# Performance work log

Hardware: AMD Instinct MI355X
Metric: run time of the kernel (lower is better)

The kernel has to match this reference:

```python
import jax, jax.numpy as jnp
import numpy as np

N_NODES = 100_000
N_EDGES = 1_600_000
D_IN, D_HID, D_OUT = 256, 64, 32
NUM_PROP = 10
ALPHA = 0.1


def setup_inputs() -> dict:
    key = jax.random.key(0)
    ks = jax.random.split(key, 8)
    features = jax.random.normal(ks[0], (N_NODES, D_IN), dtype=jnp.float32)
    row = jax.random.randint(ks[1], (N_EDGES,), 0, N_NODES, dtype=jnp.int32)
    col = jax.random.randint(ks[2], (N_EDGES,), 0, N_NODES, dtype=jnp.int32)
    # positive edge weights (stand-in for symmetric-normalized adjacency values)
    edge_vals = jax.random.uniform(ks[3], (N_EDGES,), dtype=jnp.float32) / 16.0
    W1 = jax.random.normal(ks[4], (D_IN, D_HID), dtype=jnp.float32) / np.sqrt(D_IN)
    b1 = jnp.zeros((D_HID,), dtype=jnp.float32)
    W2 = jax.random.normal(ks[5], (D_HID, D_OUT), dtype=jnp.float32) / np.sqrt(D_HID)
    b2 = jnp.zeros((D_OUT,), dtype=jnp.float32)
    return {"features": features, "row": row, "col": col, "edge_vals": edge_vals,
            "W1": W1, "b1": b1, "W2": W2, "b2": b2}


def _spmm(row, col, vals, x):
    # COO sparse-dense matmul: out[r] += vals[e] * x[col[e]] for each edge e
    return jax.ops.segment_sum(vals[:, None] * x[col], row, num_segments=N_NODES)


def reference(features, row, col, edge_vals, W1, b1, W2, b2):
    # head_transform: 2-layer MLP
    x = jax.nn.relu(features @ W1 + b1) @ W2 + b2  # [N, D_OUT]
    x0 = x
    # APPNP propagation: x = (1-alpha) * (A @ x) + alpha * x0
    def body(_, x):
        return (1.0 - ALPHA) * _spmm(row, col, edge_vals, x) + ALPHA * x0
    x = jax.lax.fori_loop(0, NUM_PROP, body, x)
    return x
```

## Files before the change

kernel.cpp:

```cpp
#include <hip/hip_runtime.h>

#define N_NODES 100000
#define N_EDGES 1600000
#define D_IN    256
#define D_HID   64
#define D_OUT   32
#define NPROP   10

#define NBUCK 196
#define CHUNK 6080
#define NCHUNK ((N_EDGES + CHUNK - 1) / CHUNK)

typedef _Float16 half_t;
typedef _Float16 h8  __attribute__((ext_vector_type(8)));
typedef _Float16 h4  __attribute__((ext_vector_type(4)));
typedef float    f4v __attribute__((ext_vector_type(4)));

__global__ __launch_bounds__(256) void pack_kernel(
    const float* __restrict__ W1, const float* __restrict__ W2,
    half_t* __restrict__ W1T, half_t* __restrict__ W2T)
{
  int t = blockIdx.x * 256 + threadIdx.x;
  if (t < 64 * 256) { int n = t >> 8, k = t & 255; W1T[t] = (half_t)W1[k * 64 + n]; }
  if (t < 32 * 64)  { int n = t >> 6, k = t & 63;  W2T[t] = (half_t)W2[k * 32 + n]; }
}

#define HSTRIDE 72

__global__ __launch_bounds__(256) void mlp_kernel(
    const float* __restrict__ F, const half_t* __restrict__ W1T,
    const float* __restrict__ b1, const half_t* __restrict__ W2T,
    const float* __restrict__ b2, half_t* __restrict__ x0h)
{
  __shared__ half_t h_lds[16 * HSTRIDE];
  __shared__ half_t out_lds[16 * 32];
  int t = threadIdx.x;
  int w = t >> 6, lane = t & 63;
  int m = lane & 15, q = lane >> 4;
  int node0 = blockIdx.x * 16;
  int hid0 = w * 16;

  f4v acc = {0.f, 0.f, 0.f, 0.f};
  const float* arow = F + (size_t)(node0 + m) * D_IN + q * 8;
  const half_t* brow = W1T + (size_t)(hid0 + m) * D_IN + q * 8;
#pragma unroll
  for (int s = 0; s < 8; ++s) {
    float4 f0 = *(const float4*)(arow + s * 32);
    float4 f1 = *(const float4*)(arow + s * 32 + 4);
    h8 a;
    a[0] = (_Float16)f0.x; a[1] = (_Float16)f0.y;
    a[2] = (_Float16)f0.z; a[3] = (_Float16)f0.w;
    a[4] = (_Float16)f1.x; a[5] = (_Float16)f1.y;
    a[6] = (_Float16)f1.z; a[7] = (_Float16)f1.w;
    h8 b = *(const h8*)(brow + s * 32);
    acc = __builtin_amdgcn_mfma_f32_16x16x32_f16(a, b, acc, 0, 0, 0);
  }

  {
    int col = hid0 + m;
    float bb = b1[col];
#pragma unroll
    for (int i = 0; i < 4; ++i) {
      float hv = fmaxf(acc[i] + bb, 0.f);
      h_lds[(q * 4 + i) * HSTRIDE + col] = (half_t)hv;
    }
  }
  __syncthreads();

  if (w < 2) {
    f4v acc2 = {0.f, 0.f, 0.f, 0.f};
    int out0 = w * 16;
#pragma unroll
    for (int s = 0; s < 2; ++s) {
      h8 a = *(const h8*)(h_lds + m * HSTRIDE + s * 32 + q * 8);
      h8 b = *(const h8*)(W2T + (size_t)(out0 + m) * D_HID + s * 32 + q * 8);
      acc2 = __builtin_amdgcn_mfma_f32_16x16x32_f16(a, b, acc2, 0, 0, 0);
    }
    int oc = out0 + m;
    float b2v = b2[oc];
#pragma unroll
    for (int i = 0; i < 4; ++i)
      out_lds[(q * 4 + i) * 32 + oc] = (half_t)(acc2[i] + b2v);
  }
  __syncthreads();

  if (t < 64) {
    int nl = t >> 2, qq = t & 3;
    *(int4*)(x0h + (size_t)(node0 + nl) * D_OUT + qq * 8) =
        *(const int4*)(out_lds + nl * 32 + qq * 8);
  }
}

__global__ __launch_bounds__(256) void bhist_kernel(
    const int* __restrict__ row, int* __restrict__ bcnt)
{
  __shared__ int lb[NBUCK];
  int t = threadIdx.x;
  for (int i = t; i < NBUCK; i += 256) lb[i] = 0;
  __syncthreads();
  int stride = gridDim.x * 256;
  for (int e = blockIdx.x * 256 + t; e < N_EDGES; e += stride)
    atomicAdd(&lb[row[e] >> 9], 1);
  __syncthreads();
  for (int i = t; i < NBUCK; i += 256)
    if (lb[i]) atomicAdd(&bcnt[i], lb[i]);
}

__global__ __launch_bounds__(256) void bscan_kernel(
    const int* __restrict__ bcnt, int* __restrict__ bbase, int* __restrict__ pbase)
{
  __shared__ int l1[256], l2[256];
  int t = threadIdx.x;
  int a = (t < NBUCK) ? bcnt[t] : 0;
  int r = (t < NBUCK) ? (((a + 3) & ~3) + 3 * 512) : 0;
  l1[t] = a; l2[t] = r;
  __syncthreads();
  for (int off = 1; off < 256; off <<= 1) {
    int x1 = (t >= off) ? l1[t - off] : 0;
    int x2 = (t >= off) ? l2[t - off] : 0;
    __syncthreads();
    l1[t] += x1; l2[t] += x2;
    __syncthreads();
  }
  if (t < NBUCK) { bbase[t] = l1[t] - a; pbase[t] = l2[t] - r; }
  if (t == NBUCK - 1) { bbase[NBUCK] = l1[t]; pbase[NBUCK] = l2[t]; }
}

__global__ __launch_bounds__(256) void bscatter_kernel(
    const int* __restrict__ row, const int* __restrict__ col,
    const float* __restrict__ vals, int* __restrict__ bfill,
    const int* __restrict__ bbase, int2* __restrict__ ebuck)
{
  __shared__ int2 img[CHUNK];
  __shared__ unsigned short sbk[CHUNK];
  __shared__ int cnt[NBUCK], base[NBUCK], gb[NBUCK], fil[NBUCK];
  __shared__ int ssc[256];
  int t = threadIdx.x;
  int e0 = blockIdx.x * CHUNK;
  int n = min(CHUNK, N_EDGES - e0);

  for (int i = t; i < NBUCK; i += 256) { cnt[i] = 0; fil[i] = 0; }
  __syncthreads();
  for (int i = t; i < n; i += 256) atomicAdd(&cnt[row[e0 + i] >> 9], 1);
  __syncthreads();
  int c = (t < NBUCK) ? cnt[t] : 0;
  ssc[t] = c;
  __syncthreads();
  for (int off = 1; off < 256; off <<= 1) {
    int add = (t >= off) ? ssc[t - off] : 0;
    __syncthreads();
    ssc[t] += add;
    __syncthreads();
  }
  if (t < NBUCK) {
    base[t] = ssc[t] - c;
    gb[t] = c ? atomicAdd(&bfill[t], c) : 0;
  }
  __syncthreads();
  for (int i = t; i < n; i += 256) {
    int r = row[e0 + i];
    int bk = r >> 9;
    int p = base[bk] + atomicAdd(&fil[bk], 1);
    img[p] = make_int2(col[e0 + i] | ((r & 511) << 17),
                       __float_as_int(vals[e0 + i]));
    sbk[p] = (unsigned short)bk;
  }
  __syncthreads();
  for (int i = t; i < n; i += 256) {
    int bk = sbk[i];
    ebuck[bbase[bk] + gb[bk] + (i - base[bk])] = img[i];
  }
}

__global__ __launch_bounds__(256) void bsort_kernel(
    const int* __restrict__ bbase, const int* __restrict__ pbase,
    const int2* __restrict__ ebuck, int2* __restrict__ epack,
    int* __restrict__ row_ptr)
{
  __shared__ int acnt[512], loff[513], lfill[512], ssc[256];
  int b = blockIdx.x, t = threadIdx.x;
  int r0 = b * 512;
  int nr = min(512, N_NODES - r0);
  int eb = bbase[b];
  int ne = bbase[b + 1] - eb;
  int pb = pbase[b];

  acnt[t] = 0; acnt[t + 256] = 0;
  lfill[t] = 0; lfill[t + 256] = 0;
  __syncthreads();
  for (int i = t; i < ne; i += 256)
    atomicAdd(&acnt[((unsigned)ebuck[eb + i].x) >> 17], 1);
  __syncthreads();
  int i0 = 2 * t, i1 = 2 * t + 1;
  int a0 = acnt[i0], a1 = acnt[i1];
  int p0 = (a0 + 3) & ~3, p1 = (a1 + 3) & ~3;
  int s = p0 + p1;
  ssc[t] = s;
  __syncthreads();
  for (int off = 1; off < 256; off <<= 1) {
    int add = (t >= off) ? ssc[t - off] : 0;
    __syncthreads();
    ssc[t] += add;
    __syncthreads();
  }
  int ex = ssc[t] - s;
  loff[i0] = ex;
  loff[i1] = ex + p0;
  if (t == 255) loff[512] = ssc[255];
  __syncthreads();
  int T = ssc[255];
  int slack = (pbase[b + 1] - pb) - T;
  int units = min(slack >> 2, nr);
  if (i0 < nr) row_ptr[r0 + i0] = pb + loff[i0] + 4 * min(i0, units);
  if (i1 < nr) row_ptr[r0 + i1] = pb + loff[i1] + 4 * min(i1, units);
  if (b == NBUCK - 1 && t == 0)
    row_ptr[N_NODES] = pb + loff[nr] + 4 * units;
  __syncthreads();
  for (int i = t; i < ne; i += 256) {
    int2 ed = ebuck[eb + i];
    int lr = ((unsigned)ed.x) >> 17;
    int cl = ed.x & 0x1FFFF;
    int p = loff[lr] + 4 * min(lr, units) + atomicAdd(&lfill[lr], 1);
    epack[pb + p] = make_int2(cl, ed.y);
  }
  __syncthreads();
  for (int i = t; i < nr; i += 256) {
    int a = acnt[i];
    int size_i = ((a + 3) & ~3) + 4 * (i < units);
    int st = loff[i] + 4 * min(i, units);
    for (int p = st + a; p < st + size_i; ++p)
      epack[pb + p] = make_int2(0, 0);
  }
}

__global__ __launch_bounds__(256) void spmm_kernel(
    const int* __restrict__ rp, const int2* __restrict__ ep,
    const half_t* __restrict__ xin, const half_t* __restrict__ x0h,
    half_t* __restrict__ xout, float* __restrict__ fout, int last)
{
  int gt = blockIdx.x * 256 + threadIdx.x;
  int r = gt >> 3;
  int c4 = (gt & 7) * 4;
  if (r >= N_NODES) return;
  int e0 = rp[r], e1 = rp[r + 1];

  float acc[4] = {0.f, 0.f, 0.f, 0.f};
  for (int e = e0; e < e1; e += 4) {
    int2 p0 = ep[e];
    int2 p1 = ep[e + 1];
    int2 p2 = ep[e + 2];
    int2 p3 = ep[e + 3];
    h4 g0 = *(const h4*)(xin + (size_t)p0.x * D_OUT + c4);
    h4 g1 = *(const h4*)(xin + (size_t)p1.x * D_OUT + c4);
    h4 g2 = *(const h4*)(xin + (size_t)p2.x * D_OUT + c4);
    h4 g3 = *(const h4*)(xin + (size_t)p3.x * D_OUT + c4);
    float v0 = __int_as_float(p0.y);
    float v1 = __int_as_float(p1.y);
    float v2 = __int_as_float(p2.y);
    float v3 = __int_as_float(p3.y);
#pragma unroll
    for (int j = 0; j < 4; ++j) {
      acc[j] = fmaf(v0, (float)g0[j], acc[j]);
      acc[j] = fmaf(v1, (float)g1[j], acc[j]);
      acc[j] = fmaf(v2, (float)g2[j], acc[j]);
      acc[j] = fmaf(v3, (float)g3[j], acc[j]);
    }
  }

  h4 x0v = *(const h4*)(x0h + (size_t)r * D_OUT + c4);
  if (last) {
    float4 o;
    o.x = 0.9f * acc[0] + 0.1f * (float)x0v[0];
    o.y = 0.9f * acc[1] + 0.1f * (float)x0v[1];
    o.z = 0.9f * acc[2] + 0.1f * (float)x0v[2];
    o.w = 0.9f * acc[3] + 0.1f * (float)x0v[3];
    *(float4*)(fout + (size_t)r * D_OUT + c4) = o;
  } else {
    h4 o;
#pragma unroll
    for (int j = 0; j < 4; ++j)
      o[j] = (half_t)(0.9f * acc[j] + 0.1f * (float)x0v[j]);
    *(h4*)(xout + (size_t)r * D_OUT + c4) = o;
  }
}

extern "C" void kernel_launch(void* const* d_in, const int* in_sizes, int n_in,
                              void* d_out, int out_size, void* d_ws, size_t ws_size,
                              hipStream_t stream) {
  const float* F     = (const float*)d_in[0];
  const int*   row   = (const int*)  d_in[1];
  const int*   col   = (const int*)  d_in[2];
  const float* evals = (const float*)d_in[3];
  const float* W1    = (const float*)d_in[4];
  const float* b1    = (const float*)d_in[5];
  const float* W2    = (const float*)d_in[6];
  const float* b2    = (const float*)d_in[7];
  float* out = (float*)d_out;

  char* w = (char*)d_ws;
  half_t* x0h    = (half_t*)(w);
  half_t* P      = (half_t*)(w +  6400000);
  half_t* Q      = (half_t*)(w + 12800000);
  int2*   ebuck  = (int2*)  (w +  6400000);
  int2*   epack  = (int2*)  (w + 19200000);
  int*   row_ptr = (int*)   (w + 34600192);
  int*   bcnt    = (int*)   (w + 35000576);
  int*   bfill   = (int*)   (w + 35001600);
  int*   bbase   = (int*)   (w + 35002624);
  int*   pbase   = (int*)   (w + 35003648);
  half_t* W1T    = (half_t*)(w + 35004672);
  half_t* W2T    = (half_t*)(w + 35037440);

  pack_kernel<<<64, 256, 0, stream>>>(W1, W2, W1T, W2T);
  mlp_kernel<<<N_NODES / 16, 256, 0, stream>>>(F, W1T, b1, W2T, b2, x0h);

  hipMemsetAsync(bcnt, 0, 2048, stream);
  bhist_kernel<<<640, 256, 0, stream>>>(row, bcnt);
  bscan_kernel<<<1, 256, 0, stream>>>(bcnt, bbase, pbase);
  bscatter_kernel<<<NCHUNK, 256, 0, stream>>>(row, col, evals, bfill, bbase, ebuck);
  bsort_kernel<<<NBUCK, 256, 0, stream>>>(bbase, pbase, ebuck, epack, row_ptr);

  const int grid_spmm = (N_NODES * 8 + 255) / 256;
  for (int i = 0; i < NPROP; ++i) {
    const half_t* xin = (i == 0) ? x0h : ((i & 1) ? P : Q);
    half_t* xout = (i & 1) ? Q : P;
    int last = (i == NPROP - 1);
    spmm_kernel<<<grid_spmm, 256, 0, stream>>>(
        row_ptr, epack, xin, x0h, xout, out, last);
  }
}
```

Before: 557.8 us.

## Split propagation into two 16-column halves and compress edges to 32 bits

The 32-wide fp16 feature matrix is split into two 16-column planes. Each half runs its own 10-step propagation, so the gathered working set per pass is half the size and more likely to stay cached. Each edge is packed into one 32-bit word: a 17-bit column and a 15-bit fp16 weight with the sign bit dropped. This halves edge traffic, costs weight precision, and relies on the weights being positive. The spmm loop is unrolled by 8 with nontemporal loads, and the MLP now handles 64 nodes per block with all four waves computing. The cost is twice as many spmm launches, and the edge list is read in both halves.

Measured after the change: 705.2 us. 26.4% more time.

```diff
diff --git a/kernel.cpp b/kernel.cpp
--- a/kernel.cpp
+++ b/kernel.cpp
@@ -15,6 +15,9 @@
 typedef _Float16 h8  __attribute__((ext_vector_type(8)));
 typedef _Float16 h4  __attribute__((ext_vector_type(4)));
 typedef float    f4v __attribute__((ext_vector_type(4)));
+typedef unsigned long long u64;
+
+union u16h { unsigned short s; half_t h; };
 
 __global__ __launch_bounds__(256) void pack_kernel(
     const float* __restrict__ W1, const float* __restrict__ W2,
@@ -25,69 +28,89 @@
   if (t < 32 * 64)  { int n = t >> 6, k = t & 63;  W2T[t] = (half_t)W2[k * 32 + n]; }
 }
 
-#define HSTRIDE 72
-
 __global__ __launch_bounds__(256) void mlp_kernel(
     const float* __restrict__ F, const half_t* __restrict__ W1T,
     const float* __restrict__ b1, const half_t* __restrict__ W2T,
-    const float* __restrict__ b2, half_t* __restrict__ x0h)
-{
-  __shared__ half_t h_lds[16 * HSTRIDE];
-  __shared__ half_t out_lds[16 * 32];
+    const float* __restrict__ b2, half_t* __restrict__ x0L,
+    half_t* __restrict__ x0H)
+{
+  __shared__ half_t h_lds[64 * 72];
+  __shared__ half_t out_lds[64 * 32];
   int t = threadIdx.x;
   int w = t >> 6, lane = t & 63;
   int m = lane & 15, q = lane >> 4;
-  int node0 = blockIdx.x * 16;
-  int hid0 = w * 16;
-
-  f4v acc = {0.f, 0.f, 0.f, 0.f};
-  const float* arow = F + (size_t)(node0 + m) * D_IN + q * 8;
-  const half_t* brow = W1T + (size_t)(hid0 + m) * D_IN + q * 8;
+  int nodeb = blockIdx.x * 64;
+  int node0 = nodeb + w * 16;
+  int nc = min(node0 + m, N_NODES - 1);
+  const float* arow = F + (size_t)nc * D_IN + q * 8;
+
+  float4 fa[16];
 #pragma unroll
   for (int s = 0; s < 8; ++s) {
-    float4 f0 = *(const float4*)(arow + s * 32);
-    float4 f1 = *(const float4*)(arow + s * 32 + 4);
+    fa[2 * s]     = *(const float4*)(arow + s * 32);
+    fa[2 * s + 1] = *(const float4*)(arow + s * 32 + 4);
+  }
+
+  f4v acc[4];
+#pragma unroll
+  for (int g = 0; g < 4; ++g) acc[g] = (f4v){0.f, 0.f, 0.f, 0.f};
+
+#pragma unroll
+  for (int s = 0; s < 8; ++s) {
+    float4 f0 = fa[2 * s], f1 = fa[2 * s + 1];
     h8 a;
     a[0] = (_Float16)f0.x; a[1] = (_Float16)f0.y;
     a[2] = (_Float16)f0.z; a[3] = (_Float16)f0.w;
     a[4] = (_Float16)f1.x; a[5] = (_Float16)f1.y;
     a[6] = (_Float16)f1.z; a[7] = (_Float16)f1.w;
-    h8 b = *(const h8*)(brow + s * 32);
-    acc = __builtin_amdgcn_mfma_f32_16x16x32_f16(a, b, acc, 0, 0, 0);
-  }
+#pragma unroll
+    for (int g = 0; g < 4; ++g) {
+      h8 b = *(const h8*)(W1T + (size_t)(g * 16 + m) * D_IN + s * 32 + q * 8);
+      acc[g] = __builtin_amdgcn_mfma_f32_16x16x32_f16(a, b, acc[g], 0, 0, 0);
+    }
+  }
+
+#pragma unroll
+  for (int g = 0; g < 4; ++g) {
+    float bb = b1[g * 16 + m];
+#pragma unroll
+    for (int i = 0; i < 4; ++i)
+      h_lds[(w * 16 + q * 4 + i) * 72 + g * 16 + m] =
+          (half_t)fmaxf(acc[g][i] + bb, 0.f);
+  }
+  __syncthreads();
+
+  f4v acc2[2];
+  acc2[0] = (f4v){0.f, 0.f, 0.f, 0.f};
+  acc2[1] = (f4v){0.f, 0.f, 0.f, 0.f};
+#pragma unroll
+  for (int s = 0; s < 2; ++s) {
+    h8 a = *(const h8*)(h_lds + (w * 16 + m) * 72 + s * 32 + q * 8);
+#pragma unroll
+    for (int g = 0; g < 2; ++g) {
+      h8 b = *(const h8*)(W2T + (size_t)(g * 16 + m) * D_HID + s * 32 + q * 8);
+      acc2[g] = __builtin_amdgcn_mfma_f32_16x16x32_f16(a, b, acc2[g], 0, 0, 0);
+    }
+  }
+#pragma unroll
+  for (int g = 0; g < 2; ++g) {
+    float b2v = b2[g * 16 + m];
+#pragma unroll
+    for (int i = 0; i < 4; ++i)
+      out_lds[(w * 16 + q * 4 + i) * 32 + g * 16 + m] = (half_t)(acc2[g][i] + b2v);
+  }
+  __syncthreads();
 
   {
-    int col = hid0 + m;
-    float bb = b1[col];
-#pragma unroll
-    for (int i = 0; i < 4; ++i) {
-      float hv = fmaxf(acc[i] + bb, 0.f);
-      h_lds[(q * 4 + i) * HSTRIDE + col] = (half_t)hv;
-    }
-  }
-  __syncthreads();
-
-  if (w < 2) {
-    f4v acc2 = {0.f, 0.f, 0.f, 0.f};
-    int out0 = w * 16;
-#pragma unroll
-    for (int s = 0; s < 2; ++s) {
-      h8 a = *(const h8*)(h_lds + m * HSTRIDE + s * 32 + q * 8);
-      h8 b = *(const h8*)(W2T + (size_t)(out0 + m) * D_HID + s * 32 + q * 8);
-      acc2 = __builtin_amdgcn_mfma_f32_16x16x32_f16(a, b, acc2, 0, 0, 0);
-    }
-    int oc = out0 + m;
-    float b2v = b2[oc];
-#pragma unroll
-    for (int i = 0; i < 4; ++i)
-      out_lds[(q * 4 + i) * 32 + oc] = (half_t)(acc2[i] + b2v);
-  }
-  __syncthreads();
-
-  if (t < 64) {
     int nl = t >> 2, qq = t & 3;
-    *(int4*)(x0h + (size_t)(node0 + nl) * D_OUT + qq * 8) =
-        *(const int4*)(out_lds + nl * 32 + qq * 8);
+    int node = nodeb + nl;
+    if (node < N_NODES) {
+      int4 v = *(const int4*)(out_lds + nl * 32 + qq * 8);
+      if (qq < 2)
+        *(int4*)(x0L + (size_t)node * 16 + qq * 8) = v;
+      else
+        *(int4*)(x0H + (size_t)node * 16 + (qq - 2) * 8) = v;
+    }
   }
 }
 
@@ -174,7 +197,7 @@
 
 __global__ __launch_bounds__(256) void bsort_kernel(
     const int* __restrict__ bbase, const int* __restrict__ pbase,
-    const int2* __restrict__ ebuck, int2* __restrict__ epack,
+    const int2* __restrict__ ebuck, unsigned* __restrict__ epack,
     int* __restrict__ row_ptr)
 {
   __shared__ int acnt[512], loff[513], lfill[512], ssc[256];
@@ -221,7 +244,8 @@
     int lr = ((unsigned)ed.x) >> 17;
     int cl = ed.x & 0x1FFFF;
     int p = loff[lr] + 4 * min(lr, units) + atomicAdd(&lfill[lr], 1);
-    epack[pb + p] = make_int2(cl, ed.y);
+    u16h cv; cv.h = (half_t)__int_as_float(ed.y);
+    epack[pb + p] = ((unsigned)cl << 15) | (unsigned)(cv.s & 0x7FFF);
   }
   __syncthreads();
   for (int i = t; i < nr; i += 256) {
@@ -229,45 +253,78 @@
     int size_i = ((a + 3) & ~3) + 4 * (i < units);
     int st = loff[i] + 4 * min(i, units);
     for (int p = st + a; p < st + size_i; ++p)
-      epack[pb + p] = make_int2(0, 0);
+      epack[pb + p] = 0u;
   }
 }
 
 __global__ __launch_bounds__(256) void spmm_kernel(
-    const int* __restrict__ rp, const int2* __restrict__ ep,
-    const half_t* __restrict__ xin, const half_t* __restrict__ x0h,
+    const int* __restrict__ rp, const unsigned* __restrict__ ep,
+    const half_t* __restrict__ xin,
+    const half_t* __restrict__ x0h,
     half_t* __restrict__ xout, float* __restrict__ fout, int last)
 {
   int gt = blockIdx.x * 256 + threadIdx.x;
-  int r = gt >> 3;
-  int c4 = (gt & 7) * 4;
+  int r = gt >> 2;
+  int c4 = (gt & 3) * 4;
   if (r >= N_NODES) return;
   int e0 = rp[r], e1 = rp[r + 1];
 
   float acc[4] = {0.f, 0.f, 0.f, 0.f};
-  for (int e = e0; e < e1; e += 4) {
-    int2 p0 = ep[e];
-    int2 p1 = ep[e + 1];
-    int2 p2 = ep[e + 2];
-    int2 p3 = ep[e + 3];
-    h4 g0 = *(const h4*)(xin + (size_t)p0.x * D_OUT + c4);
-    h4 g1 = *(const h4*)(xin + (size_t)p1.x * D_OUT + c4);
-    h4 g2 = *(const h4*)(xin + (size_t)p2.x * D_OUT + c4);
-    h4 g3 = *(const h4*)(xin + (size_t)p3.x * D_OUT + c4);
-    float v0 = __int_as_float(p0.y);
-    float v1 = __int_as_float(p1.y);
-    float v2 = __int_as_float(p2.y);
-    float v3 = __int_as_float(p3.y);
+  int e = e0;
+  for (; e + 7 < e1; e += 8) {
+    unsigned u0 = __builtin_nontemporal_load(ep + e);
+    unsigned u1 = __builtin_nontemporal_load(ep + e + 1);
+    unsigned u2 = __builtin_nontemporal_load(ep + e + 2);
+    unsigned u3 = __builtin_nontemporal_load(ep + e + 3);
+    unsigned u4 = __builtin_nontemporal_load(ep + e + 4);
+    unsigned u5 = __builtin_nontemporal_load(ep + e + 5);
+    unsigned u6 = __builtin_nontemporal_load(ep + e + 6);
+    unsigned u7 = __builtin_nontemporal_load(ep + e + 7);
+    h4 g0 = *(const h4*)(xin + (size_t)(u0 >> 15) * 16 + c4);
+    h4 g1 = *(const h4*)(xin + (size_t)(u1 >> 15) * 16 + c4);
+    h4 g2 = *(const h4*)(xin + (size_t)(u2 >> 15) * 16 + c4);
+    h4 g3 = *(const h4*)(xin + (size_t)(u3 >> 15) * 16 + c4);
+    h4 g4 = *(const h4*)(xin + (size_t)(u4 >> 15) * 16 + c4);
+    h4 g5 = *(const h4*)(xin + (size_t)(u5 >> 15) * 16 + c4);
+    h4 g6 = *(const h4*)(xin + (size_t)(u6 >> 15) * 16 + c4);
+    h4 g7 = *(const h4*)(xin + (size_t)(u7 >> 15) * 16 + c4);
+    u16h v0, v1, v2, v3, v4, v5, v6, v7;
+    v0.s = u0 & 0x7FFF; v1.s = u1 & 0x7FFF; v2.s = u2 & 0x7FFF; v3.s = u3 & 0x7FFF;
+    v4.s = u4 & 0x7FFF; v5.s = u5 & 0x7FFF; v6.s = u6 & 0x7FFF; v7.s = u7 & 0x7FFF;
 #pragma unroll
     for (int j = 0; j < 4; ++j) {
-      acc[j] = fmaf(v0, (float)g0[j], acc[j]);
-      acc[j] = fmaf(v1, (float)g1[j], acc[j]);
-      acc[j] = fmaf(v2, (float)g2[j], acc[j]);
-      acc[j] = fmaf(v3, (float)g3[j], acc[j]);
-    }
-  }
-
-  h4 x0v = *(const h4*)(x0h + (size_t)r * D_OUT + c4);
+      acc[j] = fmaf((float)v0.h, (float)g0[j], acc[j]);
+      acc[j] = fmaf((float)v1.h, (float)g1[j], acc[j]);
+      acc[j] = fmaf((float)v2.h, (float)g2[j], acc[j]);
+      acc[j] = fmaf((float)v3.h, (float)g3[j], acc[j]);
+      acc[j] = fmaf((float)v4.h, (float)g4[j], acc[j]);
+      acc[j] = fmaf((float)v5.h, (float)g5[j], acc[j]);
+      acc[j] = fmaf((float)v6.h, (float)g6[j], acc[j]);
+      acc[j] = fmaf((float)v7.h, (float)g7[j], acc[j]);
+    }
+  }
+  if (e < e1) {
+    unsigned u0 = __builtin_nontemporal_load(ep + e);
+    unsigned u1 = __builtin_nontemporal_load(ep + e + 1);
+    unsigned u2 = __builtin_nontemporal_load(ep + e + 2);
+    unsigned u3 = __builtin_nontemporal_load(ep + e + 3);
+    h4 g0 = *(const h4*)(xin + (size_t)(u0 >> 15) * 16 + c4);
+    h4 g1 = *(const h4*)(xin + (size_t)(u1 >> 15) * 16 + c4);
+    h4 g2 = *(const h4*)(xin + (size_t)(u2 >> 15) * 16 + c4);
+    h4 g3 = *(const h4*)(xin + (size_t)(u3 >> 15) * 16 + c4);
+    u16h v0, v1, v2, v3;
+    v0.s = u0 & 0x7FFF; v1.s = u1 & 0x7FFF; v2.s = u2 & 0x7FFF; v3.s = u3 & 0x7FFF;
+#pragma unroll
+    for (int j = 0; j < 4; ++j) {
+      acc[j] = fmaf((float)v0.h, (float)g0[j], acc[j]);
+      acc[j] = fmaf((float)v1.h, (float)g1[j], acc[j]);
+      acc[j] = fmaf((float)v2.h, (float)g2[j], acc[j]);
+      acc[j] = fmaf((float)v3.h, (float)g3[j], acc[j]);
+    }
+  }
+
+  u64 raw = __builtin_nontemporal_load((const u64*)(x0h + (size_t)r * 16 + c4));
+  h4 x0v = *(h4*)&raw;
   if (last) {
     float4 o;
     o.x = 0.9f * acc[0] + 0.1f * (float)x0v[0];
@@ -280,7 +337,7 @@
 #pragma unroll
     for (int j = 0; j < 4; ++j)
       o[j] = (half_t)(0.9f * acc[j] + 0.1f * (float)x0v[j]);
-    *(h4*)(xout + (size_t)r * D_OUT + c4) = o;
+    *(h4*)(xout + (size_t)r * 16 + c4) = o;
   }
 }
 
@@ -298,34 +355,42 @@
   float* out = (float*)d_out;
 
   char* w = (char*)d_ws;
-  half_t* x0h    = (half_t*)(w);
-  half_t* P      = (half_t*)(w +  6400000);
-  half_t* Q      = (half_t*)(w + 12800000);
+  half_t* x0L    = (half_t*)(w);
+  half_t* x0H    = (half_t*)(w +  3200000);
+  half_t* PL     = (half_t*)(w +  6400000);
+  half_t* QL     = (half_t*)(w +  9600000);
+  half_t* PH     = (half_t*)(w + 12800000);
+  half_t* QH     = (half_t*)(w + 16000000);
   int2*   ebuck  = (int2*)  (w +  6400000);
-  int2*   epack  = (int2*)  (w + 19200000);
-  int*   row_ptr = (int*)   (w + 34600192);
-  int*   bcnt    = (int*)   (w + 35000576);
-  int*   bfill   = (int*)   (w + 35001600);
-  int*   bbase   = (int*)   (w + 35002624);
-  int*   pbase   = (int*)   (w + 35003648);
-  half_t* W1T    = (half_t*)(w + 35004672);
-  half_t* W2T    = (half_t*)(w + 35037440);
+  unsigned* epack= (unsigned*)(w + 19200000);
+  int*   row_ptr = (int*)   (w + 26900224);
+  int*   bcnt    = (int*)   (w + 27300352);
+  int*   bfill   = (int*)   (w + 27301376);
+  int*   bbase   = (int*)   (w + 27302400);
+  int*   pbase   = (int*)   (w + 27303424);
+  half_t* W1T    = (half_t*)(w + 27304448);
+  half_t* W2T    = (half_t*)(w + 27337216);
 
   pack_kernel<<<64, 256, 0, stream>>>(W1, W2, W1T, W2T);
-  mlp_kernel<<<N_NODES / 16, 256, 0, stream>>>(F, W1T, b1, W2T, b2, x0h);
-
-  hipMemsetAsync(bcnt, 0, 2048, stream);
+  mlp_kernel<<<(N_NODES + 63) / 64, 256, 0, stream>>>(F, W1T, b1, W2T, b2, x0L, x0H);
+
+  (void)hipMemsetAsync(bcnt, 0, 2048, stream);
   bhist_kernel<<<640, 256, 0, stream>>>(row, bcnt);
   bscan_kernel<<<1, 256, 0, stream>>>(bcnt, bbase, pbase);
   bscatter_kernel<<<NCHUNK, 256, 0, stream>>>(row, col, evals, bfill, bbase, ebuck);
   bsort_kernel<<<NBUCK, 256, 0, stream>>>(bbase, pbase, ebuck, epack, row_ptr);
 
-  const int grid_spmm = (N_NODES * 8 + 255) / 256;
-  for (int i = 0; i < NPROP; ++i) {
-    const half_t* xin = (i == 0) ? x0h : ((i & 1) ? P : Q);
-    half_t* xout = (i & 1) ? Q : P;
-    int last = (i == NPROP - 1);
-    spmm_kernel<<<grid_spmm, 256, 0, stream>>>(
-        row_ptr, epack, xin, x0h, xout, out, last);
-  }
-}
+  const int grid_spmm = (N_NODES * 4 + 255) / 256;
+  for (int h = 0; h < 2; ++h) {
+    const half_t* x0h = h ? x0H : x0L;
+    half_t* Ph = h ? PH : PL;
+    half_t* Qh = h ? QH : QL;
+    float* fo = out + h * 16;
+    for (int i = 0; i < NPROP; ++i) {
+      const half_t* xin = (i == 0) ? x0h : ((i & 1) ? Ph : Qh);
+      half_t* xout = (i & 1) ? Qh : Ph;
+      spmm_kernel<<<grid_spmm, 256, 0, stream>>>(
+          row_ptr, epack, xin, x0h, xout, fo, i == NPROP - 1);
+    }
+  }
+}
```
